# Performance work log

Hardware: AMD Instinct MI355X
Metric: run time of the kernel (lower is better)

The kernel has to match this reference:

```python
import jax, jax.numpy as jnp
import numpy as np

N, IN_DIM, E_RAW, N_GRAPHS, HEADS = 50000, 128, 800000, 256, 2
NEG_ATT, NEG_ACT, EPS = 0.2, 0.01, 1e-5


def _gat(x, src, dst, W, a_src, a_dst, bias):
    # PyG GATConv: x' = xW per head; alpha = softmax_over_dst(leaky_relu(a_s.h_src + a_d.h_dst, 0.2))
    H, C = a_src.shape
    n = x.shape[0]
    h = (x @ W).reshape(n, H, C)                                  # [N,H,C]
    al_s = jnp.einsum('nhc,hc->nh', h, a_src)                     # [N,H]
    al_d = jnp.einsum('nhc,hc->nh', h, a_dst)                     # [N,H]
    e = jax.nn.leaky_relu(al_s[src] + al_d[dst], NEG_ATT)         # [E,H]
    m = jax.ops.segment_max(e, dst, num_segments=n)               # per-dst max (stable softmax)
    ee = jnp.exp(e - m[dst])
    s = jax.ops.segment_sum(ee, dst, num_segments=n)
    alpha = ee / (s[dst] + 1e-16)                                 # [E,H]
    out = jax.ops.segment_sum(h[src] * alpha[:, :, None], dst, num_segments=n)
    return out.reshape(n, H * C) + bias


def _bn(x, g, b):
    # training-mode BatchNorm1d over nodes (biased variance), eps=1e-5
    m = jnp.mean(x, 0)
    v = jnp.var(x, 0)
    return (x - m) * jax.lax.rsqrt(v + EPS) * g + b


def setup_inputs() -> dict:
    key = jax.random.key(0)
    ks = jax.random.split(key, 20)
    H, C1, C2, C3 = HEADS, 32, 64, 128
    rn = lambda i, sh, s=0.05: jax.random.normal(ks[i], sh, jnp.float32) * s
    inp = dict(
        x=jax.random.normal(ks[0], (N, IN_DIM), jnp.float32),
        edge_index=jax.random.randint(ks[1], (2, E_RAW), 0, N, jnp.int32),
        edge_weigth=jax.random.uniform(ks[2], (E_RAW,), jnp.float32),
        batch=jnp.sort(jax.random.randint(ks[3], (N,), 0, N_GRAPHS, jnp.int32)),
        W1=rn(4, (IN_DIM, H * C1)), a_src1=rn(5, (H, C1)), a_dst1=rn(6, (H, C1)),
        b1=jnp.zeros((H * C1,), jnp.float32), g1=jnp.ones((H * C1,), jnp.float32), be1=jnp.zeros((H * C1,), jnp.float32),
        W2=rn(7, (H * C1, H * C2)), a_src2=rn(8, (H, C2)), a_dst2=rn(9, (H, C2)),
        b2=jnp.zeros((H * C2,), jnp.float32), g2=jnp.ones((H * C2,), jnp.float32), be2=jnp.zeros((H * C2,), jnp.float32),
        W3=rn(10, (H * C2, H * C3)), a_src3=rn(11, (H, C3)), a_dst3=rn(12, (H, C3)),
        b3=jnp.zeros((H * C3,), jnp.float32), g3=jnp.ones((H * C3,), jnp.float32), be3=jnp.zeros((H * C3,), jnp.float32),
        Wc1=rn(13, (H * C1 + H * C2 + H * C3, 128)), bc1=jnp.zeros((128,), jnp.float32),
        Wc2=rn(14, (128, 64)), bc2=jnp.zeros((64,), jnp.float32),
        Wc3=rn(15, (64, 2)), bc3=jnp.zeros((2,), jnp.float32),
    )
    return inp


def reference(x, edge_index, edge_weigth, batch,
              W1, a_src1, a_dst1, b1, g1, be1,
              W2, a_src2, a_dst2, b2, g2, be2,
              W3, a_src3, a_dst3, b3, g3, be3,
              Wc1, bc1, Wc2, bc2, Wc3, bc3):
    n = x.shape[0]
    loops = jnp.arange(n, dtype=edge_index.dtype)  # GATConv add_self_loops=True
    src = jnp.concatenate([edge_index[0], loops])
    dst = jnp.concatenate([edge_index[1], loops])
    lr = lambda t: jax.nn.leaky_relu(t, NEG_ACT)
    x1 = lr(_bn(_gat(x, src, dst, W1, a_src1, a_dst1, b1), g1, be1))
    x2 = lr(_bn(_gat(x1, src, dst, W2, a_src2, a_dst2, b2), g2, be2))
    x3 = lr(_bn(_gat(x2, src, dst, W3, a_src3, a_dst3, b3), g3, be3))
    p = jnp.concatenate([
        jax.ops.segment_sum(x1, batch, num_segments=N_GRAPHS),
        jax.ops.segment_sum(x2, batch, num_segments=N_GRAPHS),
        jax.ops.segment_sum(x3, batch, num_segments=N_GRAPHS)], axis=1)
    h = lr(p @ Wc1 + bc1)
    h = lr(h @ Wc2 + bc2)
    return h @ Wc3 + bc3
```

## Files before the change

kernel.cpp:

```cpp
#include <hip/hip_runtime.h>
#include <hip/hip_fp16.h>
#include <math.h>

#define N_NODES 50000
#define E_RAW_N 800000
#define E_TOT   (E_RAW_N + N_NODES)
#define NGRAPH  256
#define POOL_F  448
#define SCAN_B  196
#define NSLICE  4
#define MBLK    391
#define EBLK    3321
#define PBLK    391

using f16x8 = __attribute__((ext_vector_type(8))) _Float16;
using f32x4 = __attribute__((ext_vector_type(4))) float;


template<int K, int F>
__device__ void do_wt(const float* __restrict__ W, __half* __restrict__ WT, int blk) {
    int i = blk * 256 + threadIdx.x;
    if (i >= F * (K / 8)) return;
    int f = i / (K / 8);
    int kb = (i % (K / 8)) * 8;
    __half tmp[8];
#pragma unroll
    for (int j = 0; j < 8; ++j) tmp[j] = __float2half(W[(size_t)(kb + j) * F + f]);
    *reinterpret_cast<uint4*>(WT + (size_t)f * K + kb) = *reinterpret_cast<uint4*>(tmp);
}


__global__ void k_init(int* __restrict__ deg, float* __restrict__ p,
                       float* __restrict__ bn,
                       const float* __restrict__ W1, const float* __restrict__ W2,
                       const float* __restrict__ W3, __half* __restrict__ WT1,
                       __half* __restrict__ WT2, __half* __restrict__ WT3) {
    int b = blockIdx.x;
    if (b < 448) {
        int i = b * 256 + threadIdx.x;
        if (i < N_NODES) deg[i] = 0;
        if (i < NGRAPH * POOL_F) p[i] = 0.f;
        if (i < NSLICE * 512 * 3) bn[i] = 0.f;
    } else {
        int wb = b - 448;
        if (wb < 4)       do_wt<128, 64>(W1, WT1, wb);
        else if (wb < 8)  do_wt<64, 128>(W2, WT2, wb - 4);
        else              do_wt<128, 256>(W3, WT3, wb - 8);
    }
}


__device__ inline void degrank_body(int bid, const int* __restrict__ dst_raw,
                                    int* __restrict__ deg, int* __restrict__ rank) {
    int e = bid * 256 + threadIdx.x;
    if (e >= E_TOT) return;
    int d = (e < E_RAW_N) ? dst_raw[e] : (e - E_RAW_N);
    rank[e] = atomicAdd(&deg[d], 1);
}

__global__ void k_scan1(const int* __restrict__ deg, int* __restrict__ bsum) {
    __shared__ int red[256];
    int i = blockIdx.x * 256 + threadIdx.x;
    int v = (i < N_NODES) ? deg[i] : 0;
    red[threadIdx.x] = v;
    __syncthreads();
    for (int o = 128; o > 0; o >>= 1) {
        if (threadIdx.x < o) red[threadIdx.x] += red[threadIdx.x + o];
        __syncthreads();
    }
    if (threadIdx.x == 0) bsum[blockIdx.x] = red[0];
}

__global__ void k_scan3(const int* __restrict__ deg, const int* __restrict__ bsum,
                        int* __restrict__ rowstart) {
    __shared__ int pre[256];
    __shared__ int s[256];
    int tid = threadIdx.x;
    pre[tid] = (tid < (int)blockIdx.x) ? bsum[tid] : 0;
    int i = blockIdx.x * 256 + tid;
    int v = (i < N_NODES) ? deg[i] : 0;
    s[tid] = v;
    __syncthreads();
    for (int o = 128; o > 0; o >>= 1) {
        if (tid < o) pre[tid] += pre[tid + o];
        __syncthreads();
    }
    for (int o = 1; o < 256; o <<= 1) {
        int t = (tid >= o) ? s[tid - o] : 0;
        __syncthreads();
        s[tid] += t;
        __syncthreads();
    }
    if (i < N_NODES) rowstart[i] = pre[0] + s[tid] - v;
    if (i == 0) rowstart[N_NODES] = E_TOT;
}

__global__ void k_fill(const int* __restrict__ ei, const int* __restrict__ rowstart,
                       const int* __restrict__ rank, int* __restrict__ adj) {
    int e = blockIdx.x * blockDim.x + threadIdx.x;
    if (e >= E_TOT) return;
    int s, d;
    if (e < E_RAW_N) { s = ei[e]; d = ei[E_RAW_N + e]; }
    else             { s = d = e - E_RAW_N; }
    adj[rowstart[d] + rank[e]] = s;
}


template<int F>
__device__ void bnpool_body(int bid, const __half* __restrict__ x,
                            const float* __restrict__ bnP, const float* __restrict__ g,
                            const float* __restrict__ be, const int* __restrict__ batch,
                            float* __restrict__ p, int poff) {
    constexpr int F2 = F / 2;
    constexpr int NGRP = 512 / F;
    constexpr int NPB = 128;
    int f2 = threadIdx.x % F2;
    int grp = threadIdx.x / F2;
    int f = 2 * f2;
    const float invN = 1.f / (float)N_NODES;
    float sm0 = 0.f, sm1 = 0.f, sq0 = 0.f, sq1 = 0.f;
#pragma unroll
    for (int s = 0; s < NSLICE; ++s) {
        sm0 += bnP[s * 2 * F + f];     sm1 += bnP[s * 2 * F + f + 1];
        sq0 += bnP[s * 2 * F + F + f]; sq1 += bnP[s * 2 * F + F + f + 1];
    }
    float m0 = sm0 * invN, m1 = sm1 * invN;
    float v0 = sq0 * invN - m0 * m0;
    float v1 = sq1 * invN - m1 * m1;
    float sc0 = rsqrtf(v0 + 1e-5f) * g[f];
    float sc1 = rsqrtf(v1 + 1e-5f) * g[f + 1];
    float bb0 = be[f] - m0 * sc0;
    float bb1 = be[f + 1] - m1 * sc1;
    int n0 = bid * NPB;
    int nend = n0 + NPB; if (nend > N_NODES) nend = N_NODES;
    int n = n0 + grp;
    if (n >= nend) return;
    float p0 = 0.f, p1 = 0.f;
    int cg = batch[n];
    for (; n < nend; n += NGRP) {
        float2 xv = __half22float2(*reinterpret_cast<const __half2*>(x + (size_t)n * F + f));
        float y0 = xv.x * sc0 + bb0; y0 = y0 > 0.f ? y0 : 0.01f * y0;
        float y1 = xv.y * sc1 + bb1; y1 = y1 > 0.f ? y1 : 0.01f * y1;
        int bg = batch[n];
        if (bg != cg) {
            atomicAdd(&p[cg * POOL_F + poff + f], p0);
            atomicAdd(&p[cg * POOL_F + poff + f + 1], p1);
            p0 = p1 = 0.f; cg = bg;
        }
        p0 += y0; p1 += y1;
    }
    atomicAdd(&p[cg * POOL_F + poff + f], p0);
    atomicAdd(&p[cg * POOL_F + poff + f + 1], p1);
}

template<int F>
__global__ void k_bnpool(const __half* __restrict__ x, const float* __restrict__ bnP,
                         const float* __restrict__ g, const float* __restrict__ be,
                         const int* __restrict__ batch, float* __restrict__ p, int poff) {
    bnpool_body<F>(blockIdx.x, x, bnP, g, be, batch, p, poff);
}


template<int K, int F, bool BNIN, bool SPLIT, typename TIN, typename TOUT, int SIDE>
__global__ void __launch_bounds__(256) k_mfma(
        const TIN* __restrict__ x, const __half* __restrict__ WT,
        const float* __restrict__ bnP,
        const float* __restrict__ g, const float* __restrict__ be,
        const float* __restrict__ a_src, const float* __restrict__ a_dst,
        void* __restrict__ hout, float* __restrict__ al_s, float* __restrict__ al_d,
        const int* __restrict__ dst_raw, int* __restrict__ deg, int* __restrict__ rank,
        const int* __restrict__ batch, float* __restrict__ pp, int poff) {
    if constexpr (SIDE == 1) {
        if (blockIdx.x >= MBLK) { degrank_body(blockIdx.x - MBLK, dst_raw, deg, rank); return; }
    } else if constexpr (SIDE == 2) {
        if (blockIdx.x >= MBLK) {
            if (blockIdx.y == 0)
                bnpool_body<K>(blockIdx.x - MBLK, (const __half*)x, bnP, g, be, batch, pp, poff);
            return;
        }
    }
    constexpr int FH = SPLIT ? F / 2 : F;
    constexpr int NF = FH / 16;
    constexpr int KS = K / 32;
    constexpr int MT = 2;
    constexpr int C  = F / 2;
    const int hd  = SPLIT ? (int)blockIdx.y : 0;
    const int fof = hd * C;
    __shared__ float scs[K], bbs[K];
    int tid = threadIdx.x;
    if constexpr (BNIN) {
        const float invN = 1.f / (float)N_NODES;
        for (int i = tid; i < K; i += 256) {
            float sm = 0.f, sq = 0.f;
#pragma unroll
            for (int s = 0; s < NSLICE; ++s) {
                sm += bnP[s * 2 * K + i];
                sq += bnP[s * 2 * K + K + i];
            }
            float mean = sm * invN;
            float var  = sq * invN - mean * mean;
            float sc = rsqrtf(var + 1e-5f) * g[i];
            scs[i] = sc;
            bbs[i] = be[i] - mean * sc;
        }
        __syncthreads();
    }
    int wave = tid >> 6, lane = tid & 63;
    int col = lane & 15;
    int kg  = lane >> 4;
    long n_base = ((long)blockIdx.x * 4 + wave) * (MT * 16);
    if (n_base >= N_NODES) return;

    f32x4 acc[MT][NF];
#pragma unroll
    for (int m = 0; m < MT; ++m)
#pragma unroll
        for (int t = 0; t < NF; ++t) acc[m][t] = (f32x4){0.f, 0.f, 0.f, 0.f};

    for (int ks = 0; ks < KS; ++ks) {
        int kb = ks * 32 + kg * 8;
        f16x8 af[MT];
#pragma unroll
        for (int m = 0; m < MT; ++m) {
            long nrow = n_base + m * 16 + col;
            if (nrow >= N_NODES) nrow = N_NODES - 1;
            if constexpr (sizeof(TIN) == 2) {
                uint4 u = *reinterpret_cast<const uint4*>((const __half*)x + nrow * K + kb);
                if constexpr (BNIN) {
                    const __half* hp = reinterpret_cast<const __half*>(&u);
                    f16x8 a;
#pragma unroll
                    for (int j = 0; j < 8; ++j) {
                        float y = __half2float(hp[j]) * scs[kb + j] + bbs[kb + j];
                        y = y > 0.f ? y : 0.01f * y;
                        a[j] = (_Float16)y;
                    }
                    af[m] = a;
                } else {
                    af[m] = *reinterpret_cast<const f16x8*>(&u);
                }
            } else {
                const float* xp = (const float*)x + nrow * K + kb;
                float4 v0 = *reinterpret_cast<const float4*>(xp);
                float4 v1 = *reinterpret_cast<const float4*>(xp + 4);
                f16x8 a;
                a[0] = (_Float16)v0.x; a[1] = (_Float16)v0.y;
                a[2] = (_Float16)v0.z; a[3] = (_Float16)v0.w;
                a[4] = (_Float16)v1.x; a[5] = (_Float16)v1.y;
                a[6] = (_Float16)v1.z; a[7] = (_Float16)v1.w;
                af[m] = a;
            }
        }
#pragma unroll
        for (int t = 0; t < NF; ++t) {
            f16x8 bf = *reinterpret_cast<const f16x8*>(WT + (size_t)(fof + t * 16 + col) * K + kb);
            acc[0][t] = __builtin_amdgcn_mfma_f32_16x16x32_f16(bf, af[0], acc[0][t], 0, 0, 0);
            if constexpr (MT > 1)
                acc[1][t] = __builtin_amdgcn_mfma_f32_16x16x32_f16(bf, af[1], acc[1][t], 0, 0, 0);
        }
    }

#pragma unroll
    for (int m = 0; m < MT; ++m) {
        int node_i = (int)(n_base + m * 16 + col);
        bool ok = node_i < N_NODES;
#pragma unroll
        for (int t = 0; t < NF; ++t) {
            int fb = fof + t * 16 + kg * 4;
            if (ok) {
                if constexpr (sizeof(TOUT) == 1) {
                    int pk0 = __builtin_amdgcn_cvt_pk_fp8_f32(acc[m][t][0], acc[m][t][1], 0, false);
                    int pk1 = __builtin_amdgcn_cvt_pk_fp8_f32(acc[m][t][2], acc[m][t][3], 0, false);
                    unsigned u = ((unsigned)pk0 & 0xffffu) | ((unsigned)pk1 << 16);
                    *reinterpret_cast<unsigned*>((unsigned char*)hout + (size_t)node_i * F + fb) = u;
                } else {
                    __half2 p0 = __floats2half2_rn(acc[m][t][0], acc[m][t][1]);
                    __half2 p1 = __floats2half2_rn(acc[m][t][2], acc[m][t][3]);
                    uint2 u;
                    u.x = *reinterpret_cast<unsigned int*>(&p0);
                    u.y = *reinterpret_cast<unsigned int*>(&p1);
                    *reinterpret_cast<uint2*>((__half*)hout + (size_t)node_i * F + fb) = u;
                }
            }
        }
        if constexpr (SPLIT) {
            float ss = 0.f, sd = 0.f;
#pragma unroll
            for (int t = 0; t < NF; ++t) {
#pragma unroll
                for (int r = 0; r < 4; ++r) {
                    int f = fof + t * 16 + kg * 4 + r;
                    ss += acc[m][t][r] * a_src[f];
                    sd += acc[m][t][r] * a_dst[f];
                }
            }
            ss += __shfl_xor(ss, 16); ss += __shfl_xor(ss, 32);
            sd += __shfl_xor(sd, 16); sd += __shfl_xor(sd, 32);
            if (kg == 0 && ok) {
                al_s[node_i * 2 + hd] = ss;
                al_d[node_i * 2 + hd] = sd;
            }
        } else {
            float ss0 = 0.f, sd0 = 0.f, ss1 = 0.f, sd1 = 0.f;
#pragma unroll
            for (int t = 0; t < NF; ++t) {
#pragma unroll
                for (int r = 0; r < 4; ++r) {
                    int f = t * 16 + kg * 4 + r;
                    float v = acc[m][t][r];
                    if (t < NF / 2) { ss0 += v * a_src[f]; sd0 += v * a_dst[f]; }
                    else            { ss1 += v * a_src[f]; sd1 += v * a_dst[f]; }
                }
            }
            ss0 += __shfl_xor(ss0, 16); ss0 += __shfl_xor(ss0, 32);
            sd0 += __shfl_xor(sd0, 16); sd0 += __shfl_xor(sd0, 32);
            ss1 += __shfl_xor(ss1, 16); ss1 += __shfl_xor(ss1, 32);
            sd1 += __shfl_xor(sd1, 16); sd1 += __shfl_xor(sd1, 32);
            if (kg == 0 && ok) {
                al_s[node_i * 2]     = ss0; al_s[node_i * 2 + 1] = ss1;
                al_d[node_i * 2]     = sd0; al_d[node_i * 2 + 1] = sd1;
            }
        }
    }
}


template<bool FP8> struct PayT;
template<> struct PayT<false> { using T = uint4; };
template<> struct PayT<true>  { using T = uint2; };

template<bool FP8>
__device__ inline void accum8(typename PayT<FP8>::T u, float ee, float acc[8]) {
    if constexpr (FP8) {
        auto f0 = __builtin_amdgcn_cvt_pk_f32_fp8(u.x, false);
        auto f1 = __builtin_amdgcn_cvt_pk_f32_fp8(u.x, true);
        auto f2 = __builtin_amdgcn_cvt_pk_f32_fp8(u.y, false);
        auto f3 = __builtin_amdgcn_cvt_pk_f32_fp8(u.y, true);
        acc[0] += ee * f0[0]; acc[1] += ee * f0[1];
        acc[2] += ee * f1[0]; acc[3] += ee * f1[1];
        acc[4] += ee * f2[0]; acc[5] += ee * f2[1];
        acc[6] += ee * f3[0]; acc[7] += ee * f3[1];
    } else {
        float2 f0 = __half22float2(*reinterpret_cast<const __half2*>(&u.x));
        float2 f1 = __half22float2(*reinterpret_cast<const __half2*>(&u.y));
        float2 f2 = __half22float2(*reinterpret_cast<const __half2*>(&u.z));
        float2 f3 = __half22float2(*reinterpret_cast<const __half2*>(&u.w));
        acc[0] += ee * f0.x; acc[1] += ee * f0.y;
        acc[2] += ee * f1.x; acc[3] += ee * f1.y;
        acc[4] += ee * f2.x; acc[5] += ee * f2.y;
        acc[6] += ee * f3.x; acc[7] += ee * f3.y;
    }
}

template<int F, int C, bool FP8>
__global__ void __launch_bounds__(256) k_gather(
        const int* __restrict__ rowstart, const int* __restrict__ adj,
        const void* __restrict__ hv, const float* __restrict__ al_s,
        const float* __restrict__ al_d, const float* __restrict__ bias,
        __half* __restrict__ xpre) {
    using LT = typename PayT<FP8>::T;
    constexpr int HPL = 8;
    constexpr int LPE = F / HPL;
    constexpr int EPI = 64 / LPE;
    constexpr int UNR = (EPI >= 8) ? 4 : (16 / EPI);
    constexpr int STEP = UNR * EPI;
    constexpr unsigned RSH = (F == 64 ? 6u : (F == 128 ? 7u : 8u)) + (FP8 ? 0u : 1u);
    int wave = (blockIdx.x * 256 + threadIdx.x) >> 6;
    int lane = threadIdx.x & 63;
    if (wave >= N_NODES) return;
    int n = wave;
    int rs = rowstart[n], re = rowstart[n + 1];
    float2 aldv = *reinterpret_cast<const float2*>(al_d + n * 2);

    const int es = lane / LPE;
    const int fl = lane % LPE;
    const unsigned fi = fl * HPL;
    const int hd = (fi >= C) ? 1 : 0;
    const char* base = (const char*)hv;
    const char* alsb = (const char*)al_s;
    const unsigned fioff = FP8 ? fi : fi * 2;

    const int ek  = lane & 31;
    const int ehd = lane >> 5;
    const float aldOwn = ehd ? aldv.y : aldv.x;

    float acc[HPL];
#pragma unroll
    for (int j = 0; j < HPL; ++j) acc[j] = 0.f;
    float seh = 0.f;

    int nsteps = (re - rs + STEP - 1) / STEP;

    auto mkEE = [&](unsigned s, int ib) -> float {
        float als = 0.f;
        if (ek < STEP)
            als = *reinterpret_cast<const float*>(alsb + ((s << 3) | (unsigned)(ehd << 2)));
        float v = als + aldOwn;
        v = v > 0.f ? v : 0.2f * v;
        v = fminf(v, 80.f);
        return ((ib + ek) < re && ek < STEP) ? __expf(v) : 0.f;
    };

    unsigned sOwn = (unsigned)adj[min(rs + ek, re - 1)];
    float eeOwn = mkEE(sOwn, rs);

    for (int t = 0; t < nsteps; ++t) {
        int ibase = rs + t * STEP;
        unsigned sCur = sOwn;
        float eeCur = eeOwn;
        if (t + 1 < nsteps) {
            sOwn = (unsigned)adj[min(ibase + STEP + ek, re - 1)];
            eeOwn = mkEE(sOwn, ibase + STEP);
        }
        unsigned sU[UNR];
#pragma unroll
        for (int u = 0; u < UNR; ++u)
            sU[u] = (unsigned)__shfl((int)sCur, u * EPI + es);
        LT hvU[UNR];
#pragma unroll
        for (int u = 0; u < UNR; ++u)
            hvU[u] = *reinterpret_cast<const LT*>(base + ((size_t)(sU[u] << RSH) + fioff));
        float eeU[UNR];
#pragma unroll
        for (int u = 0; u < UNR; ++u)
            eeU[u] = __shfl(eeCur, (hd << 5) | (u * EPI + es));
#pragma unroll
        for (int u = 0; u < UNR; ++u) {
            seh += eeU[u];
            accum8<FP8>(hvU[u], eeU[u], acc);
        }
    }

#pragma unroll
    for (int o = LPE; o < 64; o <<= 1) {
        seh += __shfl_xor(seh, o);
#pragma unroll
        for (int j = 0; j < HPL; ++j) acc[j] += __shfl_xor(acc[j], o);
    }

    if (es == 0) {
        float inv = 1.f / (seh + 1e-16f);
        const float* bp = bias + fi;
        __half2 o0 = __floats2half2_rn(acc[0] * inv + bp[0], acc[1] * inv + bp[1]);
        __half2 o1 = __floats2half2_rn(acc[2] * inv + bp[2], acc[3] * inv + bp[3]);
        __half2 o2 = __floats2half2_rn(acc[4] * inv + bp[4], acc[5] * inv + bp[5]);
        __half2 o3 = __floats2half2_rn(acc[6] * inv + bp[6], acc[7] * inv + bp[7]);
        uint4 u;
        u.x = *reinterpret_cast<unsigned int*>(&o0);
        u.y = *reinterpret_cast<unsigned int*>(&o1);
        u.z = *reinterpret_cast<unsigned int*>(&o2);
        u.w = *reinterpret_cast<unsigned int*>(&o3);
        *reinterpret_cast<uint4*>(xpre + (size_t)n * F + fi) = u;
    }
}


template<int F>
__global__ void __launch_bounds__(256) k_bnstats(const __half* __restrict__ x,
        float* __restrict__ bnP) {
    constexpr int SLOTS = F / 8;
    constexpr int RPI   = 256 / SLOTS;
    __shared__ float ls[256][8];
    int tid = threadIdx.x;
    int slot = tid % SLOTS;
    int r0 = tid / SLOTS;
    int slice = blockIdx.x & (NSLICE - 1);
    float s[8], q[8];
#pragma unroll
    for (int j = 0; j < 8; ++j) { s[j] = 0.f; q[j] = 0.f; }
    int stride = gridDim.x * RPI;
    for (int n = blockIdx.x * RPI + r0; n < N_NODES; n += stride) {
        uint4 u = *reinterpret_cast<const uint4*>(x + (size_t)n * F + slot * 8);
        float2 f0 = __half22float2(*reinterpret_cast<__half2*>(&u.x));
        float2 f1 = __half22float2(*reinterpret_cast<__half2*>(&u.y));
        float2 f2 = __half22float2(*reinterpret_cast<__half2*>(&u.z));
        float2 f3 = __half22float2(*reinterpret_cast<__half2*>(&u.w));
        float v[8] = {f0.x, f0.y, f1.x, f1.y, f2.x, f2.y, f3.x, f3.y};
#pragma unroll
        for (int j = 0; j < 8; ++j) { s[j] += v[j]; q[j] += v[j] * v[j]; }
    }
#pragma unroll
    for (int j = 0; j < 8; ++j) ls[tid][j] = s[j];
    __syncthreads();
    if (tid < F) {
        int sl = tid / 8, j = tid % 8;
        float t = 0.f;
        for (int r = 0; r < RPI; ++r) t += ls[r * SLOTS + sl][j];
        atomicAdd(&bnP[slice * 2 * F + tid], t);
    }
    __syncthreads();
#pragma unroll
    for (int j = 0; j < 8; ++j) ls[tid][j] = q[j];
    __syncthreads();
    if (tid < F) {
        int sl = tid / 8, j = tid % 8;
        float t = 0.f;
        for (int r = 0; r < RPI; ++r) t += ls[r * SLOTS + sl][j];
        atomicAdd(&bnP[slice * 2 * F + F + tid], t);
    }
}


__global__ void k_mlp(const float* __restrict__ p, const float* __restrict__ Wc1,
                      const float* __restrict__ bc1, const float* __restrict__ Wc2,
                      const float* __restrict__ bc2, const float* __restrict__ Wc3,
                      const float* __restrict__ bc3, float* __restrict__ out) {
    __shared__ float pr[POOL_F];
    __shared__ float h1[128];
    __shared__ float h2[64];
    int g = blockIdx.x, tid = threadIdx.x;
    for (int i = tid; i < POOL_F; i += 128) pr[i] = p[g * POOL_F + i];
    __syncthreads();
    float a = bc1[tid];
    for (int k = 0; k < POOL_F; ++k) a += pr[k] * Wc1[k * 128 + tid];
    a = a > 0.f ? a : 0.01f * a;
    h1[tid] = a;
    __syncthreads();
    if (tid < 64) {
        float b = bc2[tid];
        for (int k = 0; k < 128; ++k) b += h1[k] * Wc2[k * 64 + tid];
        b = b > 0.f ? b : 0.01f * b;
        h2[tid] = b;
    }
    __syncthreads();
    if (tid < 2) {
        float c = bc3[tid];
        for (int k = 0; k < 64; ++k) c += h2[k] * Wc3[k * 2 + tid];
        out[g * 2 + tid] = c;
    }
}


extern "C" void kernel_launch(void* const* d_in, const int* in_sizes, int n_in,
                              void* d_out, int out_size, void* d_ws, size_t ws_size,
                              hipStream_t stream) {
    const float* x    = (const float*)d_in[0];
    const int*   ei   = (const int*)d_in[1];
    const int*   batch= (const int*)d_in[3];
    const float* W1  = (const float*)d_in[4];
    const float* as1 = (const float*)d_in[5];
    const float* ad1 = (const float*)d_in[6];
    const float* b1  = (const float*)d_in[7];
    const float* g1  = (const float*)d_in[8];
    const float* be1 = (const float*)d_in[9];
    const float* W2  = (const float*)d_in[10];
    const float* as2 = (const float*)d_in[11];
    const float* ad2 = (const float*)d_in[12];
    const float* b2  = (const float*)d_in[13];
    const float* g2  = (const float*)d_in[14];
    const float* be2 = (const float*)d_in[15];
    const float* W3  = (const float*)d_in[16];
    const float* as3 = (const float*)d_in[17];
    const float* ad3 = (const float*)d_in[18];
    const float* b3  = (const float*)d_in[19];
    const float* g3  = (const float*)d_in[20];
    const float* be3 = (const float*)d_in[21];
    const float* Wc1 = (const float*)d_in[22];
    const float* bc1 = (const float*)d_in[23];
    const float* Wc2 = (const float*)d_in[24];
    const float* bc2 = (const float*)d_in[25];
    const float* Wc3 = (const float*)d_in[26];
    const float* bc3 = (const float*)d_in[27];
    float* out = (float*)d_out;

    char* wsb = (char*)d_ws;
    size_t off = 0;
    auto alloc = [&](size_t b) -> void* {
        void* pp = wsb + off;
        off += (b + 255) & ~(size_t)255;
        return pp;
    };
    int*    adj      = (int*)alloc((size_t)E_TOT * 4);
    int*    rank     = (int*)alloc((size_t)E_TOT * 4);
    int*    rowstart = (int*)alloc((size_t)(N_NODES + 1) * 4);
    int*    deg      = (int*)alloc((size_t)N_NODES * 4);
    int*    bsum     = (int*)alloc(256 * 4);
    float*  al_s     = (float*)alloc((size_t)N_NODES * 2 * 4);
    float*  al_d     = (float*)alloc((size_t)N_NODES * 2 * 4);
    float*  bn1      = (float*)alloc(NSLICE * 512 * 4);
    float*  bn2      = (float*)alloc(NSLICE * 512 * 4);
    float*  bn3      = (float*)alloc(NSLICE * 512 * 4);
    float*  p        = (float*)alloc((size_t)NGRAPH * POOL_F * 4);
    __half* WT1      = (__half*)alloc((size_t)64 * 128 * 2);
    __half* WT2      = (__half*)alloc((size_t)128 * 64 * 2);
    __half* WT3      = (__half*)alloc((size_t)256 * 128 * 2);
    __half* hbuf     = (__half*)alloc((size_t)N_NODES * 256 * 2);
    __half* xbuf     = (__half*)alloc((size_t)N_NODES * 256 * 2);

    k_init<<<472, 256, 0, stream>>>(deg, p, bn1, W1, W2, W3, WT1, WT2, WT3);

    int wb = (N_NODES + 3) / 4;
    const int sb = 480;

    k_mfma<128, 64, false, false, float, __half, 1><<<MBLK + EBLK, 256, 0, stream>>>(
        x, WT1, nullptr, nullptr, nullptr, as1, ad1, hbuf, al_s, al_d,
        ei + E_RAW_N, deg, rank, nullptr, nullptr, 0);
    k_scan1<<<SCAN_B, 256, 0, stream>>>(deg, bsum);
    k_scan3<<<SCAN_B, 256, 0, stream>>>(deg, bsum, rowstart);
    k_fill<<<EBLK, 256, 0, stream>>>(ei, rowstart, rank, adj);

    k_gather<64, 32, false><<<wb, 256, 0, stream>>>(rowstart, adj, hbuf, al_s, al_d, b1, xbuf);
    k_bnstats<64><<<sb, 256, 0, stream>>>(xbuf, bn1);

    k_mfma<64, 128, true, true, __half, __half, 2><<<dim3(MBLK + PBLK, 2), 256, 0, stream>>>(
        xbuf, WT2, bn1, g1, be1, as2, ad2, hbuf, al_s, al_d,
        nullptr, nullptr, nullptr, batch, p, 0);
    k_gather<128, 64, false><<<wb, 256, 0, stream>>>(rowstart, adj, hbuf, al_s, al_d, b2, xbuf);
    k_bnstats<128><<<sb, 256, 0, stream>>>(xbuf, bn2);

    k_mfma<128, 256, true, true, __half, __half, 2><<<dim3(MBLK + PBLK, 2), 256, 0, stream>>>(
        xbuf, WT3, bn2, g2, be2, as3, ad3, hbuf, al_s, al_d,
        nullptr, nullptr, nullptr, batch, p, 64);
    k_gather<256, 128, false><<<wb, 256, 0, stream>>>(rowstart, adj, hbuf, al_s, al_d, b3, xbuf);
    k_bnstats<256><<<sb, 256, 0, stream>>>(xbuf, bn3);

    k_bnpool<256><<<PBLK, 256, 0, stream>>>(xbuf, bn3, g3, be3, batch, p, 192);
    k_mlp<<<NGRAPH, 128, 0, stream>>>(p, Wc1, bc1, Wc2, bc2, Wc3, bc3, out);
}
```

Measured before the change: 300.8 us.

## Split layer 2/3 GAT gathers per head across a second grid dimension

Replaces the generic gather with a specialized layer-1 kernel and a per-head gather kernel for layers 2 and 3, launched with a grid y-dimension of two heads. Each wave now handles one head's channels, so more edges are processed per load step and every lane computes the attention exponent for its own head, removing the cross-half shuffle. This doubles the wave count and re-reads the adjacency and row bounds per head, trading extra index traffic for more parallelism. The unused FP8 payload path is also removed.

Result: slower. 310.7 us (+3.3%).

```diff
diff --git a/kernel.cpp b/kernel.cpp
--- a/kernel.cpp
+++ b/kernel.cpp
@@ -161,13 +161,13 @@
 }
 
 
-template<int K, int F, bool BNIN, bool SPLIT, typename TIN, typename TOUT, int SIDE>
+template<int K, int F, bool BNIN, bool SPLIT, typename TIN, int SIDE>
 __global__ void __launch_bounds__(256) k_mfma(
         const TIN* __restrict__ x, const __half* __restrict__ WT,
         const float* __restrict__ bnP,
         const float* __restrict__ g, const float* __restrict__ be,
         const float* __restrict__ a_src, const float* __restrict__ a_dst,
-        void* __restrict__ hout, float* __restrict__ al_s, float* __restrict__ al_d,
+        __half* __restrict__ hout, float* __restrict__ al_s, float* __restrict__ al_d,
         const int* __restrict__ dst_raw, int* __restrict__ deg, int* __restrict__ rank,
         const int* __restrict__ batch, float* __restrict__ pp, int poff) {
     if constexpr (SIDE == 1) {
@@ -268,19 +268,12 @@
         for (int t = 0; t < NF; ++t) {
             int fb = fof + t * 16 + kg * 4;
             if (ok) {
-                if constexpr (sizeof(TOUT) == 1) {
-                    int pk0 = __builtin_amdgcn_cvt_pk_fp8_f32(acc[m][t][0], acc[m][t][1], 0, false);
-                    int pk1 = __builtin_amdgcn_cvt_pk_fp8_f32(acc[m][t][2], acc[m][t][3], 0, false);
-                    unsigned u = ((unsigned)pk0 & 0xffffu) | ((unsigned)pk1 << 16);
-                    *reinterpret_cast<unsigned*>((unsigned char*)hout + (size_t)node_i * F + fb) = u;
-                } else {
-                    __half2 p0 = __floats2half2_rn(acc[m][t][0], acc[m][t][1]);
-                    __half2 p1 = __floats2half2_rn(acc[m][t][2], acc[m][t][3]);
-                    uint2 u;
-                    u.x = *reinterpret_cast<unsigned int*>(&p0);
-                    u.y = *reinterpret_cast<unsigned int*>(&p1);
-                    *reinterpret_cast<uint2*>((__half*)hout + (size_t)node_i * F + fb) = u;
-                }
+                __half2 p0 = __floats2half2_rn(acc[m][t][0], acc[m][t][1]);
+                __half2 p1 = __floats2half2_rn(acc[m][t][2], acc[m][t][3]);
+                uint2 u;
+                u.x = *reinterpret_cast<unsigned int*>(&p0);
+                u.y = *reinterpret_cast<unsigned int*>(&p1);
+                *reinterpret_cast<uint2*>(hout + (size_t)node_i * F + fb) = u;
             }
         }
         if constexpr (SPLIT) {
@@ -325,46 +318,24 @@
 }
 
 
-template<bool FP8> struct PayT;
-template<> struct PayT<false> { using T = uint4; };
-template<> struct PayT<true>  { using T = uint2; };
-
-template<bool FP8>
-__device__ inline void accum8(typename PayT<FP8>::T u, float ee, float acc[8]) {
-    if constexpr (FP8) {
-        auto f0 = __builtin_amdgcn_cvt_pk_f32_fp8(u.x, false);
-        auto f1 = __builtin_amdgcn_cvt_pk_f32_fp8(u.x, true);
-        auto f2 = __builtin_amdgcn_cvt_pk_f32_fp8(u.y, false);
-        auto f3 = __builtin_amdgcn_cvt_pk_f32_fp8(u.y, true);
-        acc[0] += ee * f0[0]; acc[1] += ee * f0[1];
-        acc[2] += ee * f1[0]; acc[3] += ee * f1[1];
-        acc[4] += ee * f2[0]; acc[5] += ee * f2[1];
-        acc[6] += ee * f3[0]; acc[7] += ee * f3[1];
-    } else {
-        float2 f0 = __half22float2(*reinterpret_cast<const __half2*>(&u.x));
-        float2 f1 = __half22float2(*reinterpret_cast<const __half2*>(&u.y));
-        float2 f2 = __half22float2(*reinterpret_cast<const __half2*>(&u.z));
-        float2 f3 = __half22float2(*reinterpret_cast<const __half2*>(&u.w));
-        acc[0] += ee * f0.x; acc[1] += ee * f0.y;
-        acc[2] += ee * f1.x; acc[3] += ee * f1.y;
-        acc[4] += ee * f2.x; acc[5] += ee * f2.y;
-        acc[6] += ee * f3.x; acc[7] += ee * f3.y;
-    }
-}
-
-template<int F, int C, bool FP8>
-__global__ void __launch_bounds__(256) k_gather(
+__device__ inline void accum_h8(uint4 u, float ee, float acc[8]) {
+    float2 f0 = __half22float2(*reinterpret_cast<const __half2*>(&u.x));
+    float2 f1 = __half22float2(*reinterpret_cast<const __half2*>(&u.y));
+    float2 f2 = __half22float2(*reinterpret_cast<const __half2*>(&u.z));
+    float2 f3 = __half22float2(*reinterpret_cast<const __half2*>(&u.w));
+    acc[0] += ee * f0.x; acc[1] += ee * f0.y;
+    acc[2] += ee * f1.x; acc[3] += ee * f1.y;
+    acc[4] += ee * f2.x; acc[5] += ee * f2.y;
+    acc[6] += ee * f3.x; acc[7] += ee * f3.y;
+}
+
+__global__ void __launch_bounds__(256) k_gather1(
         const int* __restrict__ rowstart, const int* __restrict__ adj,
-        const void* __restrict__ hv, const float* __restrict__ al_s,
+        const __half* __restrict__ hv, const float* __restrict__ al_s,
         const float* __restrict__ al_d, const float* __restrict__ bias,
         __half* __restrict__ xpre) {
-    using LT = typename PayT<FP8>::T;
-    constexpr int HPL = 8;
-    constexpr int LPE = F / HPL;
-    constexpr int EPI = 64 / LPE;
-    constexpr int UNR = (EPI >= 8) ? 4 : (16 / EPI);
-    constexpr int STEP = UNR * EPI;
-    constexpr unsigned RSH = (F == 64 ? 6u : (F == 128 ? 7u : 8u)) + (FP8 ? 0u : 1u);
+    constexpr int F = 64, C = 32;
+    constexpr int HPL = 8, LPE = 8, EPI = 8, UNR = 4, STEP = 32;
     int wave = (blockIdx.x * 256 + threadIdx.x) >> 6;
     int lane = threadIdx.x & 63;
     if (wave >= N_NODES) return;
@@ -378,7 +349,6 @@
     const int hd = (fi >= C) ? 1 : 0;
     const char* base = (const char*)hv;
     const char* alsb = (const char*)al_s;
-    const unsigned fioff = FP8 ? fi : fi * 2;
 
     const int ek  = lane & 31;
     const int ehd = lane >> 5;
@@ -392,13 +362,11 @@
     int nsteps = (re - rs + STEP - 1) / STEP;
 
     auto mkEE = [&](unsigned s, int ib) -> float {
-        float als = 0.f;
-        if (ek < STEP)
-            als = *reinterpret_cast<const float*>(alsb + ((s << 3) | (unsigned)(ehd << 2)));
+        float als = *reinterpret_cast<const float*>(alsb + ((s << 3) | (unsigned)(ehd << 2)));
         float v = als + aldOwn;
         v = v > 0.f ? v : 0.2f * v;
         v = fminf(v, 80.f);
-        return ((ib + ek) < re && ek < STEP) ? __expf(v) : 0.f;
+        return ((ib + ek) < re) ? __expf(v) : 0.f;
     };
 
     unsigned sOwn = (unsigned)adj[min(rs + ek, re - 1)];
@@ -413,21 +381,21 @@
             eeOwn = mkEE(sOwn, ibase + STEP);
         }
         unsigned sU[UNR];
+        uint4 hvU[UNR];
+        float eeU[UNR];
 #pragma unroll
         for (int u = 0; u < UNR; ++u)
             sU[u] = (unsigned)__shfl((int)sCur, u * EPI + es);
-        LT hvU[UNR];
 #pragma unroll
         for (int u = 0; u < UNR; ++u)
-            hvU[u] = *reinterpret_cast<const LT*>(base + ((size_t)(sU[u] << RSH) + fioff));
-        float eeU[UNR];
+            hvU[u] = *reinterpret_cast<const uint4*>(base + (((size_t)sU[u] << 7) + fi * 2));
 #pragma unroll
         for (int u = 0; u < UNR; ++u)
             eeU[u] = __shfl(eeCur, (hd << 5) | (u * EPI + es));
 #pragma unroll
         for (int u = 0; u < UNR; ++u) {
             seh += eeU[u];
-            accum8<FP8>(hvU[u], eeU[u], acc);
+            accum_h8(hvU[u], eeU[u], acc);
         }
     }
 
@@ -451,6 +419,101 @@
         u.z = *reinterpret_cast<unsigned int*>(&o2);
         u.w = *reinterpret_cast<unsigned int*>(&o3);
         *reinterpret_cast<uint4*>(xpre + (size_t)n * F + fi) = u;
+    }
+}
+
+
+template<int CF, int FSTR>
+__global__ void __launch_bounds__(256) k_gatherH(
+        const int* __restrict__ rowstart, const int* __restrict__ adj,
+        const __half* __restrict__ hv, const float* __restrict__ al_s,
+        const float* __restrict__ al_d, const float* __restrict__ bias,
+        __half* __restrict__ xpre) {
+    constexpr int HPL = 8;
+    constexpr int LPE = CF / HPL;
+    constexpr int EPI = 64 / LPE;
+    constexpr int UNR = 4;
+    constexpr int STEP = UNR * EPI;
+    constexpr unsigned RSHB = (FSTR == 128) ? 8u : 9u;
+    int wave = (blockIdx.x * 256 + threadIdx.x) >> 6;
+    int lane = threadIdx.x & 63;
+    if (wave >= N_NODES) return;
+    int n = wave;
+    const int hd = blockIdx.y;
+    int rs = rowstart[n], re = rowstart[n + 1];
+    float ald = al_d[n * 2 + hd];
+
+    const int es = lane / LPE;
+    const int fl = lane % LPE;
+    const unsigned fo = (unsigned)(hd * CF) + fl * HPL;
+    const char* base = (const char*)hv;
+    const char* alsb = (const char*)al_s;
+
+    float acc[HPL];
+#pragma unroll
+    for (int j = 0; j < HPL; ++j) acc[j] = 0.f;
+    float seh = 0.f;
+
+    int nsteps = (re - rs + STEP - 1) / STEP;
+
+    auto mkEE = [&](unsigned s, int ib) -> float {
+        float als = *reinterpret_cast<const float*>(alsb + ((s << 3) | (unsigned)(hd << 2)));
+        float v = als + ald;
+        v = v > 0.f ? v : 0.2f * v;
+        v = fminf(v, 80.f);
+        return ((ib + lane) < re && lane < STEP) ? __expf(v) : 0.f;
+    };
+
+    unsigned sOwn = (unsigned)adj[min(rs + lane, re - 1)];
+    float eeOwn = mkEE(sOwn, rs);
+
+    for (int t = 0; t < nsteps; ++t) {
+        int ibase = rs + t * STEP;
+        unsigned sCur = sOwn;
+        float eeCur = eeOwn;
+        if (t + 1 < nsteps) {
+            sOwn = (unsigned)adj[min(ibase + STEP + lane, re - 1)];
+            eeOwn = mkEE(sOwn, ibase + STEP);
+        }
+        unsigned sU[UNR];
+        uint4 hvU[UNR];
+        float eeU[UNR];
+#pragma unroll
+        for (int u = 0; u < UNR; ++u)
+            sU[u] = (unsigned)__shfl((int)sCur, u * EPI + es);
+#pragma unroll
+        for (int u = 0; u < UNR; ++u)
+            hvU[u] = *reinterpret_cast<const uint4*>(base + (((size_t)sU[u] << RSHB) + fo * 2));
+#pragma unroll
+        for (int u = 0; u < UNR; ++u)
+            eeU[u] = __shfl(eeCur, u * EPI + es);
+#pragma unroll
+        for (int u = 0; u < UNR; ++u) {
+            seh += eeU[u];
+            accum_h8(hvU[u], eeU[u], acc);
+        }
+    }
+
+#pragma unroll
+    for (int o = LPE; o < 64; o <<= 1) {
+        seh += __shfl_xor(seh, o);
+#pragma unroll
+        for (int j = 0; j < HPL; ++j) acc[j] += __shfl_xor(acc[j], o);
+    }
+
+    if (es == 0) {
+        float inv = 1.f / (seh + 1e-16f);
+        const float* bp = bias + fo;
+        __half2 o0 = __floats2half2_rn(acc[0] * inv + bp[0], acc[1] * inv + bp[1]);
+        __half2 o1 = __floats2half2_rn(acc[2] * inv + bp[2], acc[3] * inv + bp[3]);
+        __half2 o2 = __floats2half2_rn(acc[4] * inv + bp[4], acc[5] * inv + bp[5]);
+        __half2 o3 = __floats2half2_rn(acc[6] * inv + bp[6], acc[7] * inv + bp[7]);
+        uint4 u;
+        u.x = *reinterpret_cast<unsigned int*>(&o0);
+        u.y = *reinterpret_cast<unsigned int*>(&o1);
+        u.z = *reinterpret_cast<unsigned int*>(&o2);
+        u.w = *reinterpret_cast<unsigned int*>(&o3);
+        *reinterpret_cast<uint4*>(xpre + (size_t)n * FSTR + fo) = u;
     }
 }
 
@@ -592,26 +655,26 @@
     int wb = (N_NODES + 3) / 4;
     const int sb = 480;
 
-    k_mfma<128, 64, false, false, float, __half, 1><<<MBLK + EBLK, 256, 0, stream>>>(
+    k_mfma<128, 64, false, false, float, 1><<<MBLK + EBLK, 256, 0, stream>>>(
         x, WT1, nullptr, nullptr, nullptr, as1, ad1, hbuf, al_s, al_d,
         ei + E_RAW_N, deg, rank, nullptr, nullptr, 0);
     k_scan1<<<SCAN_B, 256, 0, stream>>>(deg, bsum);
     k_scan3<<<SCAN_B, 256, 0, stream>>>(deg, bsum, rowstart);
     k_fill<<<EBLK, 256, 0, stream>>>(ei, rowstart, rank, adj);
 
-    k_gather<64, 32, false><<<wb, 256, 0, stream>>>(rowstart, adj, hbuf, al_s, al_d, b1, xbuf);
+    k_gather1<<<wb, 256, 0, stream>>>(rowstart, adj, hbuf, al_s, al_d, b1, xbuf);
     k_bnstats<64><<<sb, 256, 0, stream>>>(xbuf, bn1);
 
-    k_mfma<64, 128, true, true, __half, __half, 2><<<dim3(MBLK + PBLK, 2), 256, 0, stream>>>(
+    k_mfma<64, 128, true, true, __half, 2><<<dim3(MBLK + PBLK, 2), 256, 0, stream>>>(
         xbuf, WT2, bn1, g1, be1, as2, ad2, hbuf, al_s, al_d,
         nullptr, nullptr, nullptr, batch, p, 0);
-    k_gather<128, 64, false><<<wb, 256, 0, stream>>>(rowstart, adj, hbuf, al_s, al_d, b2, xbuf);
+    k_gatherH<64, 128><<<dim3(wb, 2), 256, 0, stream>>>(rowstart, adj, hbuf, al_s, al_d, b2, xbuf);
     k_bnstats<128><<<sb, 256, 0, stream>>>(xbuf, bn2);
 
-    k_mfma<128, 256, true, true, __half, __half, 2><<<dim3(MBLK + PBLK, 2), 256, 0, stream>>>(
+    k_mfma<128, 256, true, true, __half, 2><<<dim3(MBLK + PBLK, 2), 256, 0, stream>>>(
         xbuf, WT3, bn2, g2, be2, as3, ad3, hbuf, al_s, al_d,
         nullptr, nullptr, nullptr, batch, p, 64);
-    k_gather<256, 128, false><<<wb, 256, 0, stream>>>(rowstart, adj, hbuf, al_s, al_d, b3, xbuf);
+    k_gatherH<128, 256><<<dim3(wb, 2), 256, 0, stream>>>(rowstart, adj, hbuf, al_s, al_d, b3, xbuf);
     k_bnstats<256><<<sb, 256, 0, stream>>>(xbuf, bn3);
 
     k_bnpool<256><<<PBLK, 256, 0, stream>>>(xbuf, bn3, g3, be3, batch, p, 192);
```
